# Performance work log

Measured on AMD Instinct MI355X. Metric: run time of the kernel, lower is better.

## Reference

```python
import jax, jax.numpy as jnp
import numpy as np

B, L, D, H, SPD = 16, 512, 768, 12, 5
DH = D // H
LN_EPS = 1e-5
CLAMP_MIN = 1e-6


def setup_inputs() -> dict:
    key = jax.random.key(0)
    ks = jax.random.split(key, 8)
    s = 1.0 / np.sqrt(D)
    return {
        "tgt": jax.random.normal(ks[0], (B, L, D), jnp.float32),
        "query_pos": jax.random.normal(ks[1], (B, L, D), jnp.float32),
        "pairwise_locs": jax.random.normal(ks[2], (B, L, L, SPD), jnp.float32),
        "Wq": jax.random.normal(ks[3], (D, D), jnp.float32) * s,
        "bq": jnp.zeros((D,), jnp.float32),
        "Wk": jax.random.normal(ks[4], (D, D), jnp.float32) * s,
        "bk": jnp.zeros((D,), jnp.float32),
        "Wv": jax.random.normal(ks[5], (D, D), jnp.float32) * s,
        "bv": jnp.zeros((D,), jnp.float32),
        "Wo": jax.random.normal(ks[6], (D, D), jnp.float32) * s,
        "bo": jnp.zeros((D,), jnp.float32),
        "Wloc": jax.random.normal(ks[7], (SPD, H), jnp.float32) * (1.0 / np.sqrt(SPD)),
        "bloc": jnp.zeros((H,), jnp.float32),
        "ln_g": jnp.ones((D,), jnp.float32),
        "ln_b": jnp.zeros((D,), jnp.float32),
    }


def _layer_norm(x, g, b):
    mu = jnp.mean(x, axis=-1, keepdims=True)
    var = jnp.mean(jnp.square(x - mu), axis=-1, keepdims=True)
    return g * (x - mu) * jax.lax.rsqrt(var + LN_EPS) + b


def reference(tgt, query_pos, pairwise_locs, Wq, bq, Wk, bk, Wv, bv, Wo, bo, Wloc, bloc, ln_g, ln_b):
    # forward_post path: q = k = tgt + query_pos; v = tgt
    qk_in = tgt + query_pos
    q = (qk_in @ Wq + bq).reshape(B, L, H, DH)   # [B,L,H,DH]
    k = (qk_in @ Wk + bk).reshape(B, L, H, DH)
    v = (tgt @ Wv + bv).reshape(B, L, H, DH)

    scale = np.float32(1.0 / np.sqrt(DH))
    attn = jnp.einsum('blhd,bthd->bhlt', q, k) * scale   # [B,H,L,L]

    # spatial fusion 'mul': relu(Linear(pairwise_locs)) -> log-domain additive bias
    loc_attn = jax.nn.relu(pairwise_locs @ Wloc + bloc)   # [B,L,L,H]
    loc_attn = jnp.transpose(loc_attn, (0, 3, 1, 2))      # [B,H,L,L]
    fused = jax.nn.softmax(jnp.log(jnp.clip(loc_attn, CLAMP_MIN, None)) + attn, axis=-1)

    out = jnp.einsum('bhlt,bthd->blhd', fused, v).reshape(B, L, D)
    out = out @ Wo + bo                                   # attn output (tgt2)

    # residual + (dropout p=0) + LayerNorm
    return _layer_norm(tgt + out, ln_g, ln_b)
```

## Files before the change

kernel.cpp:

```cpp
#include <hip/hip_runtime.h>
#include <math.h>

#define BB 16
#define LL 512
#define DD 768
#define HH 12
#define DHH 64
#define SPDD 5
#define MM (BB*LL)
#define LN_EPS 1e-5f
#define CLAMP_MINV 1e-6f

typedef __attribute__((ext_vector_type(8))) short bf8_t;
typedef __attribute__((ext_vector_type(4))) float f4_t;

__device__ __forceinline__ short f2bf(float x) {
    unsigned u = __builtin_bit_cast(unsigned, x);
    unsigned r = (u + 0x7FFFu + ((u >> 16) & 1u)) >> 16;
    return (short)r;
}
__device__ __forceinline__ float bf2f(short s) {
    unsigned u = ((unsigned)(unsigned short)s) << 16;
    return __builtin_bit_cast(float, u);
}

__device__ __forceinline__ void gld16(const short* g, short* l) {
    __builtin_amdgcn_global_load_lds(
        (const __attribute__((address_space(1))) unsigned int*)g,
        (__attribute__((address_space(3))) unsigned int*)l,
        16, 0, 0);
}

__device__ __forceinline__ float block_sum(float v, float* red, int tid) {
    #pragma unroll
    for (int off = 32; off; off >>= 1) v += __shfl_down(v, off, 64);
    __syncthreads();
    if ((tid & 63) == 0) red[tid >> 6] = v;
    __syncthreads();
    return red[0] + red[1] + red[2] + red[3];
}

template<bool PRE>
__global__ __launch_bounds__(256) void prep_kernel(
    const float* __restrict__ tgt, const float* __restrict__ qpos,
    const float* __restrict__ ploc, const float* __restrict__ Wloc,
    const float* __restrict__ bloc,
    const float* __restrict__ W0, const float* __restrict__ W1,
    const float* __restrict__ W2, const float* __restrict__ W3,
    short* __restrict__ aqk, short* __restrict__ av, short* __restrict__ la,
    short* __restrict__ O0, short* __restrict__ O1,
    short* __restrict__ O2, short* __restrict__ O3)
{
    __shared__ float T[64][65];
    const int nbias = PRE ? 2048 : 0;
    const int t = blockIdx.x;
    if (PRE && t < nbias) {
        const int g   = t * 256 + threadIdx.x;
        const int tch = g & 63;
        const int l   = (g >> 6) & 511;
        const int b   = g >> 15;
        const int t0  = tch * 8;
        float p[40];
        const float* src = ploc + (((size_t)b * LL + l) * LL + t0) * SPDD;
        #pragma unroll
        for (int i = 0; i < 10; ++i)
            *(float4*)(p + i * 4) = *(const float4*)(src + i * 4);
        #pragma unroll
        for (int h = 0; h < HH; ++h) {
            float wl[SPDD];
            #pragma unroll
            for (int s = 0; s < SPDD; ++s) wl[s] = Wloc[s * HH + h];
            const float bl = bloc[h];
            short o[8];
            #pragma unroll
            for (int i = 0; i < 8; ++i) {
                float v = bl;
                #pragma unroll
                for (int s = 0; s < SPDD; ++s) v += p[i * SPDD + s] * wl[s];
                v = fmaxf(fmaxf(v, 0.f), CLAMP_MINV);
                o[i] = f2bf(v);
            }
            *(bf8_t*)(la + (((size_t)(b * HH + h) * LL + l) * LL + t0)) = *(bf8_t*)o;
        }
    } else if (t < nbias + 3072) {
        const int cb = t - nbias;
        const size_t base = ((size_t)cb * 256 + threadIdx.x) * 8;
        const float4 t0 = *(const float4*)(tgt + base);
        const float4 t1 = *(const float4*)(tgt + base + 4);
        const float4 p0 = *(const float4*)(qpos + base);
        const float4 p1 = *(const float4*)(qpos + base + 4);
        short v[8], q[8];
        v[0] = f2bf(t0.x); v[1] = f2bf(t0.y); v[2] = f2bf(t0.z); v[3] = f2bf(t0.w);
        v[4] = f2bf(t1.x); v[5] = f2bf(t1.y); v[6] = f2bf(t1.z); v[7] = f2bf(t1.w);
        q[0] = f2bf(t0.x + p0.x); q[1] = f2bf(t0.y + p0.y);
        q[2] = f2bf(t0.z + p0.z); q[3] = f2bf(t0.w + p0.w);
        q[4] = f2bf(t1.x + p1.x); q[5] = f2bf(t1.y + p1.y);
        q[6] = f2bf(t1.z + p1.z); q[7] = f2bf(t1.w + p1.w);
        *(bf8_t*)(av + base)  = *(bf8_t*)v;
        *(bf8_t*)(aqk + base) = *(bf8_t*)q;
    } else {
        const int wt = t - (nbias + 3072);
        const int wi = wt / 144;
        const int rem = wt % 144;
        const float* W; short* O;
        switch (wi) {
            case 0: W = W0; O = O0; break;
            case 1: W = W1; O = O1; break;
            case 2: W = W2; O = O2; break;
            default: W = W3; O = O3; break;
        }
        const int n0 = (rem % 12) * 64, k0 = (rem / 12) * 64;
        const int tid = threadIdx.x;
        {
            const int kk = tid >> 4, nv = (tid & 15) * 4;
            #pragma unroll
            for (int i = 0; i < 4; ++i) {
                const int k = kk + i * 16;
                const float4 v = *(const float4*)(W + (size_t)(k0 + k) * DD + n0 + nv);
                T[k][nv + 0] = v.x; T[k][nv + 1] = v.y;
                T[k][nv + 2] = v.z; T[k][nv + 3] = v.w;
            }
        }
        __syncthreads();
        {
            const int n = tid >> 2, kc = (tid & 3) * 16;
            short tmp[16];
            #pragma unroll
            for (int i = 0; i < 16; ++i) tmp[i] = f2bf(T[kc + i][n]);
            short* dst = O + (size_t)(n0 + n) * DD + k0 + kc;
            *(bf8_t*)dst       = *(bf8_t*)tmp;
            *(bf8_t*)(dst + 8) = *(bf8_t*)(tmp + 8);
        }
    }
}

__global__ __launch_bounds__(256) void gemm_qkv(
    const short* __restrict__ Aqk, const short* __restrict__ Av,
    const short* __restrict__ Wq, const float* __restrict__ bq, short* __restrict__ oq,
    const short* __restrict__ Wk, const float* __restrict__ bk, short* __restrict__ ok,
    const short* __restrict__ Wv, const float* __restrict__ bv, short* __restrict__ ov)
{
    __shared__ short As[128 * 64];
    __shared__ short Bs[128 * 64];
    const int id = blockIdx.y * 18 + blockIdx.x;
    const int xcd = id & 7, j = id >> 3;
    const int by = xcd * 8 + j / 18;
    const int gx = j % 18;
    const int seg = gx / 6;
    const int bx = gx % 6;
    const short* A  = (seg == 2) ? Av : Aqk;
    const short* Wt = (seg == 0) ? Wq : (seg == 1) ? Wk : Wv;
    const float* bias = (seg == 0) ? bq : (seg == 1) ? bk : bv;
    short* out = (seg == 0) ? oq : (seg == 1) ? ok : ov;

    const int n0 = bx * 128, m0 = by * 128;
    const int tid = threadIdx.x;
    const int w = tid >> 6, lane = tid & 63;
    const int quad = lane >> 4, l16 = lane & 15;
    const int wm = w & 1, wn = w >> 1;
    const int sr = w * 8 + (lane >> 3);
    const int sp = lane & 7;

    f4_t acc[4][4];
    #pragma unroll
    for (int i = 0; i < 4; ++i)
        #pragma unroll
        for (int jj = 0; jj < 4; ++jj) acc[i][jj] = (f4_t){0.f, 0.f, 0.f, 0.f};

    for (int k0 = 0; k0 < DD; k0 += 64) {
        __syncthreads();
        #pragma unroll
        for (int ra = 0; ra < 4; ++ra) {
            const int r = sr + ra * 32;
            const int c = sp ^ (r & 7);
            const int ldso = ra * 2048 + w * 512 + lane * 8;
            gld16(A  + (size_t)(m0 + r) * DD + k0 + c * 8, As + ldso);
            gld16(Wt + (size_t)(n0 + r) * DD + k0 + c * 8, Bs + ldso);
        }
        __syncthreads();
        #pragma unroll
        for (int s = 0; s < 2; ++s) {
            bf8_t a[4], b[4];
            #pragma unroll
            for (int i = 0; i < 4; ++i) {
                const int rA = wm * 64 + i * 16 + l16;
                const int pA = (s * 4 + quad) ^ (rA & 7);
                a[i] = *(const bf8_t*)(As + rA * 64 + pA * 8);
                const int rB = wn * 64 + i * 16 + l16;
                const int pB = (s * 4 + quad) ^ (rB & 7);
                b[i] = *(const bf8_t*)(Bs + rB * 64 + pB * 8);
            }
            #pragma unroll
            for (int i = 0; i < 4; ++i)
                #pragma unroll
                for (int jj = 0; jj < 4; ++jj)
                    acc[i][jj] = __builtin_amdgcn_mfma_f32_16x16x32_bf16(a[i], b[jj], acc[i][jj], 0, 0, 0);
        }
    }

    float bvv[4];
    #pragma unroll
    for (int jj = 0; jj < 4; ++jj) bvv[jj] = bias[n0 + wn * 64 + jj * 16 + l16];
    #pragma unroll
    for (int i = 0; i < 4; ++i) {
        #pragma unroll
        for (int jj = 0; jj < 4; ++jj) {
            const int n = n0 + wn * 64 + jj * 16 + l16;
            #pragma unroll
            for (int r = 0; r < 4; ++r) {
                const int m = m0 + wm * 64 + i * 16 + quad * 4 + r;
                const float val = acc[i][jj][r] + bvv[jj];
                const int b_ = m >> 9, l = m & 511;
                const int h = n >> 6, d = n & 63;
                if (seg < 2)
                    out[(((size_t)(b_ * HH + h)) * LL + l) * DHH + d] = f2bf(val);
                else
                    out[(((size_t)(b_ * HH + h)) * DHH + d) * LL + l] = f2bf(val);
            }
        }
    }
}

__global__ __launch_bounds__(256) void gemm_o(
    const short* __restrict__ A, const short* __restrict__ Wt,
    const float* __restrict__ bias, float* __restrict__ out)
{
    __shared__ short As[128 * 64];
    __shared__ short Bs[128 * 64];
    const int id = blockIdx.y * 6 + blockIdx.x;
    const int xcd = id & 7, j = id >> 3;
    const int by = xcd * 8 + j / 6;
    const int bx = j % 6;
    const int n0 = bx * 128, m0 = by * 128;
    const int tid = threadIdx.x;
    const int w = tid >> 6, lane = tid & 63;
    const int quad = lane >> 4, l16 = lane & 15;
    const int wm = w & 1, wn = w >> 1;
    const int sr = w * 8 + (lane >> 3);
    const int sp = lane & 7;

    f4_t acc[4][4];
    #pragma unroll
    for (int i = 0; i < 4; ++i)
        #pragma unroll
        for (int jj = 0; jj < 4; ++jj) acc[i][jj] = (f4_t){0.f, 0.f, 0.f, 0.f};

    for (int k0 = 0; k0 < DD; k0 += 64) {
        __syncthreads();
        #pragma unroll
        for (int ra = 0; ra < 4; ++ra) {
            const int r = sr + ra * 32;
            const int c = sp ^ (r & 7);
            const int ldso = ra * 2048 + w * 512 + lane * 8;
            gld16(A  + (size_t)(m0 + r) * DD + k0 + c * 8, As + ldso);
            gld16(Wt + (size_t)(n0 + r) * DD + k0 + c * 8, Bs + ldso);
        }
        __syncthreads();
        #pragma unroll
        for (int s = 0; s < 2; ++s) {
            bf8_t a[4], b[4];
            #pragma unroll
            for (int i = 0; i < 4; ++i) {
                const int rA = wm * 64 + i * 16 + l16;
                const int pA = (s * 4 + quad) ^ (rA & 7);
                a[i] = *(const bf8_t*)(As + rA * 64 + pA * 8);
                const int rB = wn * 64 + i * 16 + l16;
                const int pB = (s * 4 + quad) ^ (rB & 7);
                b[i] = *(const bf8_t*)(Bs + rB * 64 + pB * 8);
            }
            #pragma unroll
            for (int i = 0; i < 4; ++i)
                #pragma unroll
                for (int jj = 0; jj < 4; ++jj)
                    acc[i][jj] = __builtin_amdgcn_mfma_f32_16x16x32_bf16(a[i], b[jj], acc[i][jj], 0, 0, 0);
        }
    }

    float bvv[4];
    #pragma unroll
    for (int jj = 0; jj < 4; ++jj) bvv[jj] = bias[n0 + wn * 64 + jj * 16 + l16];
    #pragma unroll
    for (int i = 0; i < 4; ++i)
        #pragma unroll
        for (int jj = 0; jj < 4; ++jj) {
            const int n = n0 + wn * 64 + jj * 16 + l16;
            #pragma unroll
            for (int r = 0; r < 4; ++r) {
                const int m = m0 + wm * 64 + i * 16 + quad * 4 + r;
                out[(size_t)m * DD + n] = acc[i][jj][r] + bvv[jj];
            }
        }
}

template<bool PRE>
__global__ __launch_bounds__(256) void attn_mfma(
    const short* __restrict__ Q, const short* __restrict__ K,
    const short* __restrict__ Vt, const short* __restrict__ LA,
    const float* __restrict__ ploc, const float* __restrict__ Wloc,
    const float* __restrict__ bloc, short* __restrict__ out)
{
    __shared__ short Ks[64 * 64];
    __shared__ short Vs[64 * 64];
    __shared__ short bs16[64 * 68];
    __shared__ short Ps[4][16 * 64];

    const int h = blockIdx.x % 12, b = blockIdx.x / 12;
    const int qt = blockIdx.y;
    const int tid = threadIdx.x;
    const int w = tid >> 6, lane = tid & 63;
    const int quad = lane >> 4, l16 = lane & 15;
    const int q0 = qt * 64;
    const size_t bh = (size_t)b * HH + h;

    float wl[SPDD];
    float blc = 0.f;
    if (!PRE) {
        #pragma unroll
        for (int s = 0; s < SPDD; ++s) wl[s] = Wloc[s * HH + h];
        blc = bloc[h];
    }

    const int qr = q0 + w * 16 + l16;
    const bf8_t aq0 = *(const bf8_t*)(Q + (bh * LL + qr) * DHH + quad * 8);
    const bf8_t aq1 = *(const bf8_t*)(Q + (bh * LL + qr) * DHH + quad * 8 + 32);

    f4_t o[4];
    #pragma unroll
    for (int dj = 0; dj < 4; ++dj) o[dj] = (f4_t){0.f, 0.f, 0.f, 0.f};
    float m_row[4], l_row[4];
    #pragma unroll
    for (int r = 0; r < 4; ++r) { m_row[r] = -1e30f; l_row[r] = 0.f; }

    const short* Kg = K  + bh * LL * DHH;
    const short* Vg = Vt + bh * DHH * LL;
    const short* Bg = PRE ? (LA + (bh * LL + q0) * LL) : nullptr;

    const int srow = tid >> 2;
    const int cb   = (tid & 3) * 2;
    const int sw   = srow & 7;

    for (int t0 = 0; t0 < LL; t0 += 64) {
        __syncthreads();
        {
            const short* src = Kg + (size_t)(t0 + srow) * DHH + cb * 8;
            *(bf8_t*)(Ks + srow * 64 + ((cb ^ sw) * 8))       = *(const bf8_t*)(src);
            *(bf8_t*)(Ks + srow * 64 + (((cb + 1) ^ sw) * 8)) = *(const bf8_t*)(src + 8);
        }
        {
            const short* src = Vg + (size_t)srow * LL + t0 + cb * 8;
            *(bf8_t*)(Vs + srow * 64 + ((cb ^ sw) * 8))       = *(const bf8_t*)(src);
            *(bf8_t*)(Vs + srow * 64 + (((cb + 1) ^ sw) * 8)) = *(const bf8_t*)(src + 8);
        }
        {
            const int l = tid >> 2, ts = (tid & 3) * 16;
            if (PRE) {
                const short* src = Bg + (size_t)l * LL + t0 + ts;
                #pragma unroll
                for (int i = 0; i < 4; ++i)
                    *(short4*)(bs16 + l * 68 + ts + i * 4) = *(const short4*)(src + i * 4);
            } else {
                const float* pp = ploc + (((size_t)b * LL + q0 + l) * LL + t0 + ts) * SPDD;
                #pragma unroll
                for (int i = 0; i < 16; ++i) {
                    float v = blc;
                    #pragma unroll
                    for (int s = 0; s < SPDD; ++s) v += pp[i * SPDD + s] * wl[s];
                    v = fmaxf(fmaxf(v, 0.f), CLAMP_MINV);
                    bs16[l * 68 + ts + i] = f2bf(v);
                }
            }
        }
        __syncthreads();

        f4_t sv[4];
        #pragma unroll
        for (int j = 0; j < 4; ++j) {
            const int rB = j * 16 + l16;
            const int x = rB & 7;
            const bf8_t b0 = *(const bf8_t*)(Ks + rB * 64 + ((quad ^ x) * 8));
            const bf8_t b1 = *(const bf8_t*)(Ks + rB * 64 + (((quad + 4) ^ x) * 8));
            f4_t c = (f4_t){0.f, 0.f, 0.f, 0.f};
            c = __builtin_amdgcn_mfma_f32_16x16x32_bf16(aq0, b0, c, 0, 0, 0);
            c = __builtin_amdgcn_mfma_f32_16x16x32_bf16(aq1, b1, c, 0, 0, 0);
            sv[j] = c;
        }
        #pragma unroll
        for (int j = 0; j < 4; ++j)
            #pragma unroll
            for (int r = 0; r < 4; ++r) sv[j][r] *= 0.125f;

        #pragma unroll
        for (int r = 0; r < 4; ++r) {
            const int lrel = w * 16 + quad * 4 + r;
            float mx = fmaxf(fmaxf(sv[0][r], sv[1][r]), fmaxf(sv[2][r], sv[3][r]));
            mx = fmaxf(mx, __shfl_xor(mx, 1, 16));
            mx = fmaxf(mx, __shfl_xor(mx, 2, 16));
            mx = fmaxf(mx, __shfl_xor(mx, 4, 16));
            mx = fmaxf(mx, __shfl_xor(mx, 8, 16));
            const float mn = fmaxf(m_row[r], mx);
            const float al = __expf(m_row[r] - mn);
            m_row[r] = mn;
            float rs = 0.f;
            #pragma unroll
            for (int j = 0; j < 4; ++j) {
                const float lav = bf2f(bs16[lrel * 68 + j * 16 + l16]);
                const float p = lav * __expf(sv[j][r] - mn);
                sv[j][r] = p;
                rs += p;
            }
            rs += __shfl_xor(rs, 1, 16);
            rs += __shfl_xor(rs, 2, 16);
            rs += __shfl_xor(rs, 4, 16);
            rs += __shfl_xor(rs, 8, 16);
            l_row[r] = l_row[r] * al + rs;
            #pragma unroll
            for (int dj = 0; dj < 4; ++dj) o[dj][r] *= al;
        }
        short* Pw = Ps[w];
        #pragma unroll
        for (int r = 0; r < 4; ++r) {
            const int rp = quad * 4 + r, rp7 = rp & 7;
            #pragma unroll
            for (int j = 0; j < 4; ++j) {
                const int t = j * 16 + l16;
                Pw[rp * 64 + (((t >> 3) ^ rp7) * 8) + (t & 7)] = f2bf(sv[j][r]);
            }
        }
        const int m7 = l16 & 7;
        const bf8_t ap0 = *(const bf8_t*)(Pw + l16 * 64 + ((quad ^ m7) * 8));
        const bf8_t ap1 = *(const bf8_t*)(Pw + l16 * 64 + (((quad + 4) ^ m7) * 8));
        #pragma unroll
        for (int dj = 0; dj < 4; ++dj) {
            const int rB = dj * 16 + l16;
            const int x = rB & 7;
            const bf8_t b0 = *(const bf8_t*)(Vs + rB * 64 + ((quad ^ x) * 8));
            const bf8_t b1 = *(const bf8_t*)(Vs + rB * 64 + (((quad + 4) ^ x) * 8));
            o[dj] = __builtin_amdgcn_mfma_f32_16x16x32_bf16(ap0, b0, o[dj], 0, 0, 0);
            o[dj] = __builtin_amdgcn_mfma_f32_16x16x32_bf16(ap1, b1, o[dj], 0, 0, 0);
        }
    }

    #pragma unroll
    for (int r = 0; r < 4; ++r) {
        const int l = q0 + w * 16 + quad * 4 + r;
        const float inv = 1.f / l_row[r];
        short* op = out + ((size_t)b * LL + l) * DD + h * DHH;
        #pragma unroll
        for (int dj = 0; dj < 4; ++dj)
            op[dj * 16 + l16] = f2bf(o[dj][r] * inv);
    }
}

__global__ __launch_bounds__(256) void ln_kernel(
    const float* __restrict__ x, const float* __restrict__ tgt,
    const float* __restrict__ g, const float* __restrict__ bta,
    float* __restrict__ out)
{
    const int row = blockIdx.x;
    const int tid = threadIdx.x;
    __shared__ float red[4];

    const float* xp = x + (size_t)row * DD;
    const float* tp = tgt + (size_t)row * DD;

    float vals[3];
    float s = 0.f;
    #pragma unroll
    for (int i = 0; i < 3; ++i) {
        const float v = xp[tid + i * 256] + tp[tid + i * 256];
        vals[i] = v;
        s += v;
    }
    s = block_sum(s, red, tid);
    const float mu = s * (1.f / 768.f);

    float vs = 0.f;
    #pragma unroll
    for (int i = 0; i < 3; ++i) {
        const float dv = vals[i] - mu;
        vs += dv * dv;
    }
    vs = block_sum(vs, red, tid);
    const float rstd = rsqrtf(vs * (1.f / 768.f) + LN_EPS);

    #pragma unroll
    for (int i = 0; i < 3; ++i) {
        const int cidx = tid + i * 256;
        out[(size_t)row * DD + cidx] = g[cidx] * (vals[i] - mu) * rstd + bta[cidx];
    }
}

extern "C" void kernel_launch(void* const* d_in, const int* in_sizes, int n_in,
                              void* d_out, int out_size, void* d_ws, size_t ws_size,
                              hipStream_t stream) {
    const float* tgt   = (const float*)d_in[0];
    const float* qpos  = (const float*)d_in[1];
    const float* ploc  = (const float*)d_in[2];
    const float* Wq    = (const float*)d_in[3];
    const float* bq    = (const float*)d_in[4];
    const float* Wk    = (const float*)d_in[5];
    const float* bk    = (const float*)d_in[6];
    const float* Wv    = (const float*)d_in[7];
    const float* bv    = (const float*)d_in[8];
    const float* Wo    = (const float*)d_in[9];
    const float* bo    = (const float*)d_in[10];
    const float* Wloc  = (const float*)d_in[11];
    const float* bloc  = (const float*)d_in[12];
    const float* ln_g  = (const float*)d_in[13];
    const float* ln_b  = (const float*)d_in[14];

    const size_t NQ = (size_t)MM * DD;
    const size_t NW = (size_t)DD * DD;
    const size_t NB = (size_t)BB * HH * LL * LL;

    short* qb   = (short*)d_ws;
    short* kb   = qb  + NQ;
    short* vtb  = kb  + NQ;
    short* aob  = vtb + NQ;
    short* aqk  = aob + NQ;
    short* av   = aqk + NQ;
    float* pbuf = (float*)aqk;
    short* wqt  = av + NQ;
    short* wkt  = wqt + NW;
    short* wvt  = wkt + NW;
    short* wot  = wvt + NW;
    short* lab  = wot + NW;

    const size_t needed = (size_t)(6 * NQ + 4 * NW + NB) * 2;
    const bool pre = (ws_size >= needed);

    if (pre)
        prep_kernel<true ><<<5696, 256, 0, stream>>>(tgt, qpos, ploc, Wloc, bloc,
                                                     Wq, Wk, Wv, Wo,
                                                     aqk, av, lab, wqt, wkt, wvt, wot);
    else
        prep_kernel<false><<<3648, 256, 0, stream>>>(tgt, qpos, ploc, Wloc, bloc,
                                                     Wq, Wk, Wv, Wo,
                                                     aqk, av, lab, wqt, wkt, wvt, wot);

    gemm_qkv<<<dim3(18, 64), 256, 0, stream>>>(aqk, av, wqt, bq, qb,
                                               wkt, bk, kb, wvt, bv, vtb);

    if (pre)
        attn_mfma<true ><<<dim3(192, 8), 256, 0, stream>>>(qb, kb, vtb, lab, ploc, Wloc, bloc, aob);
    else
        attn_mfma<false><<<dim3(192, 8), 256, 0, stream>>>(qb, kb, vtb, nullptr, ploc, Wloc, bloc, aob);

    gemm_o<<<dim3(6, 64), 256, 0, stream>>>(aob, wot, bo, pbuf);

    ln_kernel<<<MM, 256, 0, stream>>>(pbuf, tgt, ln_g, ln_b, (float*)d_out);
}
```

Baseline: 371.7 us.

## Compute location bias inside attention and remap blocks for XCD L2 locality

```diff
diff --git a/kernel.cpp b/kernel.cpp
--- a/kernel.cpp
+++ b/kernel.cpp
@@ -40,51 +40,18 @@
     return red[0] + red[1] + red[2] + red[3];
 }
 
-template<bool PRE>
 __global__ __launch_bounds__(256) void prep_kernel(
     const float* __restrict__ tgt, const float* __restrict__ qpos,
-    const float* __restrict__ ploc, const float* __restrict__ Wloc,
-    const float* __restrict__ bloc,
     const float* __restrict__ W0, const float* __restrict__ W1,
     const float* __restrict__ W2, const float* __restrict__ W3,
-    short* __restrict__ aqk, short* __restrict__ av, short* __restrict__ la,
+    short* __restrict__ aqk, short* __restrict__ av,
     short* __restrict__ O0, short* __restrict__ O1,
     short* __restrict__ O2, short* __restrict__ O3)
 {
     __shared__ float T[64][65];
-    const int nbias = PRE ? 2048 : 0;
     const int t = blockIdx.x;
-    if (PRE && t < nbias) {
-        const int g   = t * 256 + threadIdx.x;
-        const int tch = g & 63;
-        const int l   = (g >> 6) & 511;
-        const int b   = g >> 15;
-        const int t0  = tch * 8;
-        float p[40];
-        const float* src = ploc + (((size_t)b * LL + l) * LL + t0) * SPDD;
-        #pragma unroll
-        for (int i = 0; i < 10; ++i)
-            *(float4*)(p + i * 4) = *(const float4*)(src + i * 4);
-        #pragma unroll
-        for (int h = 0; h < HH; ++h) {
-            float wl[SPDD];
-            #pragma unroll
-            for (int s = 0; s < SPDD; ++s) wl[s] = Wloc[s * HH + h];
-            const float bl = bloc[h];
-            short o[8];
-            #pragma unroll
-            for (int i = 0; i < 8; ++i) {
-                float v = bl;
-                #pragma unroll
-                for (int s = 0; s < SPDD; ++s) v += p[i * SPDD + s] * wl[s];
-                v = fmaxf(fmaxf(v, 0.f), CLAMP_MINV);
-                o[i] = f2bf(v);
-            }
-            *(bf8_t*)(la + (((size_t)(b * HH + h) * LL + l) * LL + t0)) = *(bf8_t*)o;
-        }
-    } else if (t < nbias + 3072) {
-        const int cb = t - nbias;
-        const size_t base = ((size_t)cb * 256 + threadIdx.x) * 8;
+    if (t < 3072) {
+        const size_t base = ((size_t)t * 256 + threadIdx.x) * 8;
         const float4 t0 = *(const float4*)(tgt + base);
         const float4 t1 = *(const float4*)(tgt + base + 4);
         const float4 p0 = *(const float4*)(qpos + base);
@@ -99,7 +66,7 @@
         *(bf8_t*)(av + base)  = *(bf8_t*)v;
         *(bf8_t*)(aqk + base) = *(bf8_t*)q;
     } else {
-        const int wt = t - (nbias + 3072);
+        const int wt = t - 3072;
         const int wi = wt / 144;
         const int rem = wt % 144;
         const float* W; short* O;
@@ -292,10 +259,9 @@
         }
 }
 
-template<bool PRE>
 __global__ __launch_bounds__(256) void attn_mfma(
     const short* __restrict__ Q, const short* __restrict__ K,
-    const short* __restrict__ Vt, const short* __restrict__ LA,
+    const short* __restrict__ Vt,
     const float* __restrict__ ploc, const float* __restrict__ Wloc,
     const float* __restrict__ bloc, short* __restrict__ out)
 {
@@ -304,8 +270,12 @@
     __shared__ short bs16[64 * 68];
     __shared__ short Ps[4][16 * 64];
 
-    const int h = blockIdx.x % 12, b = blockIdx.x / 12;
-    const int qt = blockIdx.y;
+    const int id = blockIdx.x;
+    const int xcd = id & 7, slot = id >> 3;
+    const int b = xcd + 8 * (slot / 96);
+    const int s2 = slot % 96;
+    const int h = s2 % 12, qt = s2 / 12;
+
     const int tid = threadIdx.x;
     const int w = tid >> 6, lane = tid & 63;
     const int quad = lane >> 4, l16 = lane & 15;
@@ -313,12 +283,9 @@
     const size_t bh = (size_t)b * HH + h;
 
     float wl[SPDD];
-    float blc = 0.f;
-    if (!PRE) {
-        #pragma unroll
-        for (int s = 0; s < SPDD; ++s) wl[s] = Wloc[s * HH + h];
-        blc = bloc[h];
-    }
+    #pragma unroll
+    for (int s = 0; s < SPDD; ++s) wl[s] = Wloc[s * HH + h];
+    const float blc = bloc[h];
 
     const int qr = q0 + w * 16 + l16;
     const bf8_t aq0 = *(const bf8_t*)(Q + (bh * LL + qr) * DHH + quad * 8);
@@ -333,7 +300,6 @@
 
     const short* Kg = K  + bh * LL * DHH;
     const short* Vg = Vt + bh * DHH * LL;
-    const short* Bg = PRE ? (LA + (bh * LL + q0) * LL) : nullptr;
 
     const int srow = tid >> 2;
     const int cb   = (tid & 3) * 2;
@@ -353,22 +319,27 @@
         }
         {
             const int l = tid >> 2, ts = (tid & 3) * 16;
-            if (PRE) {
-                const short* src = Bg + (size_t)l * LL + t0 + ts;
+            const float* pp = ploc + (((size_t)b * LL + q0 + l) * LL + t0 + ts) * SPDD;
+            short o16[16];
+            #pragma unroll
+            for (int g = 0; g < 4; ++g) {
+                float4 c[5];
+                const float* src = pp + g * 20;
                 #pragma unroll
-                for (int i = 0; i < 4; ++i)
-                    *(short4*)(bs16 + l * 68 + ts + i * 4) = *(const short4*)(src + i * 4);
-            } else {
-                const float* pp = ploc + (((size_t)b * LL + q0 + l) * LL + t0 + ts) * SPDD;
+                for (int i = 0; i < 5; ++i) c[i] = *(const float4*)(src + i * 4);
+                const float* pf = (const float*)c;
                 #pragma unroll
-                for (int i = 0; i < 16; ++i) {
+                for (int e = 0; e < 4; ++e) {
                     float v = blc;
                     #pragma unroll
-                    for (int s = 0; s < SPDD; ++s) v += pp[i * SPDD + s] * wl[s];
+                    for (int s = 0; s < SPDD; ++s) v += pf[e * SPDD + s] * wl[s];
                     v = fmaxf(fmaxf(v, 0.f), CLAMP_MINV);
-                    bs16[l * 68 + ts + i] = f2bf(v);
+                    o16[g * 4 + e] = f2bf(v);
                 }
             }
+            #pragma unroll
+            for (int i = 0; i < 4; ++i)
+                *(short4*)(bs16 + l * 68 + ts + i * 4) = *(short4*)(o16 + i * 4);
         }
         __syncthreads();
 
@@ -511,7 +482,6 @@
 
     const size_t NQ = (size_t)MM * DD;
     const size_t NW = (size_t)DD * DD;
-    const size_t NB = (size_t)BB * HH * LL * LL;
 
     short* qb   = (short*)d_ws;
     short* kb   = qb  + NQ;
@@ -524,27 +494,14 @@
     short* wkt  = wqt + NW;
     short* wvt  = wkt + NW;
     short* wot  = wvt + NW;
-    short* lab  = wot + NW;
-
-    const size_t needed = (size_t)(6 * NQ + 4 * NW + NB) * 2;
-    const bool pre = (ws_size >= needed);
-
-    if (pre)
-        prep_kernel<true ><<<5696, 256, 0, stream>>>(tgt, qpos, ploc, Wloc, bloc,
-                                                     Wq, Wk, Wv, Wo,
-                                                     aqk, av, lab, wqt, wkt, wvt, wot);
-    else
-        prep_kernel<false><<<3648, 256, 0, stream>>>(tgt, qpos, ploc, Wloc, bloc,
-                                                     Wq, Wk, Wv, Wo,
-                                                     aqk, av, lab, wqt, wkt, wvt, wot);
+
+    prep_kernel<<<3648, 256, 0, stream>>>(tgt, qpos, Wq, Wk, Wv, Wo,
+                                          aqk, av, wqt, wkt, wvt, wot);
 
     gemm_qkv<<<dim3(18, 64), 256, 0, stream>>>(aqk, av, wqt, bq, qb,
                                                wkt, bk, kb, wvt, bv, vtb);
 
-    if (pre)
-        attn_mfma<true ><<<dim3(192, 8), 256, 0, stream>>>(qb, kb, vtb, lab, ploc, Wloc, bloc, aob);
-    else
-        attn_mfma<false><<<dim3(192, 8), 256, 0, stream>>>(qb, kb, vtb, nullptr, ploc, Wloc, bloc, aob);
+    attn_mfma<<<1536, 256, 0, stream>>>(qb, kb, vtb, ploc, Wloc, bloc, aob);
 
     gemm_o<<<dim3(6, 64), 256, 0, stream>>>(aob, wot, bo, pbuf);
 
```

New measurement: 392.2 us. 1.05x slower.
